# Performance work log

Measured on AMD Instinct MI355X. Metric: run time of the kernel, lower is better.

Reference implementation:

```python
import jax, jax.numpy as jnp
import numpy as np

# Sizes from init_kwargs / input_specs
D_MODEL = 1024; D_INT = 64; KW = 32; B = 2; L = 4096
SAMPLING = np.array([5, 5, 2, 1, 1]); DILATIONS = np.array([1, 1, 2, 4, 8])
SUBHEADS = len(SAMPLING); HEADS = int(SAMPLING.sum())  # 5, 14
HEAD_OF_SUB = np.repeat(np.arange(SUBHEADS), SAMPLING)  # subhead index for each head
HEAD_DIL = np.repeat(DILATIONS, SAMPLING)                # dilation for each head


def _win_idx(dil):
    # centered dilated band, clipped at sequence edges -> [L, KW]
    offs = (np.arange(KW) - KW // 2) * dil
    return np.clip(np.arange(L)[:, None] + offs[None, :], 0, L - 1)

SUB_IDX = jnp.asarray(np.stack([_win_idx(d) for d in DILATIONS]))  # [SUBHEADS, L, KW]
HEAD_IDX = jnp.asarray(np.stack([_win_idx(d) for d in HEAD_DIL]))  # [HEADS, L, KW]


def setup_inputs() -> dict:
    rng = jax.random.key(0)
    ks = jax.random.split(rng, 9)
    n = lambda i, sh, sc=1.0: jax.random.normal(ks[i], sh, dtype=jnp.float32) * sc
    return dict(
        query=n(0, (B, L, D_MODEL)),
        key=n(1, (B, L, D_MODEL)),
        value=n(2, (B, L, D_MODEL)),
        Wq=n(3, (SUBHEADS, D_MODEL, D_INT), 0.02),
        bq=jnp.zeros((SUBHEADS, D_INT), jnp.float32),
        Wk=n(4, (SUBHEADS, D_MODEL, D_INT), 0.02),
        bk=jnp.zeros((SUBHEADS, D_INT), jnp.float32),
        Wv=n(5, (HEADS, D_MODEL, D_INT), 0.02),
        bv=jnp.zeros((HEADS, D_INT), jnp.float32),
        Ws=n(6, (HEADS, KW, KW), 0.05) + jnp.eye(KW, dtype=jnp.float32)[None],
        bs=jnp.zeros((HEADS, KW), jnp.float32),
        Wc=n(7, (HEADS * D_INT, D_MODEL), 0.02),
        bc=jnp.zeros((D_MODEL,), jnp.float32),
    )


def reference(query, key, value, Wq, bq, Wk, bk, Wv, bv, Ws, bs, Wc, bc):
    # per-subhead query/key projections: [S, B, L, Di]
    q = jnp.einsum('bld,sdi->sbli', query, Wq) + bq[:, None, None, :]
    k = jnp.einsum('bld,sdi->sbli', key, Wk) + bk[:, None, None, :]
    # per-head value projection: [H, B, L, Di]
    v = jnp.einsum('bld,hdi->hbli', value, Wv) + bv[:, None, None, :]
    # dilated banded key windows per subhead: [S, B, L, KW, Di]
    kw = jax.vmap(lambda kh, ix: kh[:, ix], in_axes=(0, 0))(k, SUB_IDX)
    # banded scores [S, B, L, KW]
    scores = jnp.einsum('sbli,sblki->sblk', q, kw) / jnp.sqrt(jnp.float32(D_INT))
    # supersample: replicate each subhead's scores to its heads -> [H, B, L, KW]
    scores_h = scores[HEAD_OF_SUB]
    # per-head positional supersampling linear on the score window
    sampled = jnp.einsum('hblk,hkm->hblm', scores_h, Ws) + bs[:, None, None, :]
    attn = jax.nn.softmax(sampled, axis=-1)
    # dilated value windows per head: [H, B, L, KW, Di]
    vw = jax.vmap(lambda vh, ix: vh[:, ix], in_axes=(0, 0))(v, HEAD_IDX)
    out = jnp.einsum('hblk,hblki->hbli', attn, vw)  # [H, B, L, Di]
    out = jnp.transpose(out, (1, 2, 0, 3)).reshape(B, L, HEADS * D_INT)
    return out @ Wc + bc  # [B, L, D_MODEL]
```

## Files before the change

### kernel.cpp

```cpp
#include <hip/hip_runtime.h>
#include <math.h>

#define D_MODEL 1024
#define D_INT   64
#define KW      32
#define L_SEQ   4096
#define SUBHEADS 5
#define HEADS   14
#define M_ROWS  8192
#define N_CAT   896
#define NQK     320

typedef unsigned short us;
typedef unsigned int   uu;
typedef __attribute__((ext_vector_type(2))) unsigned int uu2;
typedef __attribute__((ext_vector_type(4))) unsigned int uu4;
typedef __attribute__((ext_vector_type(8))) short bf16x8_t;
typedef __attribute__((ext_vector_type(4))) float f32x4_t;

__device__ __forceinline__ float u2f(uu u) {
    float f; __builtin_memcpy(&f, &u, 4); return f;
}
__device__ __forceinline__ float blo(uu u) { return u2f(u << 16); }
__device__ __forceinline__ float bhi(uu u) { return u2f(u & 0xffff0000u); }
__device__ __forceinline__ us f2b(float f) {
    uu u; __builtin_memcpy(&u, &f, 4);
    u += 0x7fffu + ((u >> 16) & 1u);
    return (us)(u >> 16);
}
__device__ __forceinline__ uu pack2(float a, float b) {
    return (uu)f2b(a) | ((uu)f2b(b) << 16);
}
__device__ __forceinline__ uu cvtpk(float a, float b) {
    uu r;
    asm("v_cvt_pk_bf16_f32 %0, %1, %2" : "=v"(r) : "v"(a), "v"(b));
    return r;
}
__device__ __forceinline__ void load16(void* lds, const void* g) {
    __builtin_amdgcn_global_load_lds(
        (const __attribute__((address_space(1))) unsigned int*)g,
        (__attribute__((address_space(3))) unsigned int*)lds, 16, 0, 0);
}
__device__ __forceinline__ int subhead_of(int h) {
    return (h < 5) ? 0 : (h < 10) ? 1 : (h < 12) ? 2 : (h == 12) ? 3 : 4;
}

#define CAST_BLK 3072
__global__ __launch_bounds__(256)
void prep_kernel(const float* __restrict__ q, const float* __restrict__ k,
                 const float* __restrict__ v,
                 const float* __restrict__ Wq, const float* __restrict__ Wk,
                 const float* __restrict__ Wv, const float* __restrict__ Wc,
                 us* __restrict__ Xq, us* __restrict__ Xk, us* __restrict__ Xv,
                 us* __restrict__ Wqt, us* __restrict__ Wkt,
                 us* __restrict__ Wvt, us* __restrict__ Wct)
{
    __shared__ float t[32][33];
    const int tid = threadIdx.x;
    const int b = blockIdx.x;

    if (b < CAST_BLK) {
        const int arr = b >> 10;
        const int blk = b & 1023;
        const f32x4_t* s = (const f32x4_t*)((arr == 0) ? q : (arr == 1) ? k : v);
        uu2* d = (uu2*)((arr == 0) ? Xq : (arr == 1) ? Xk : Xv);
        const int i0 = blk * 2048 + tid;
        f32x4_t xs[8];
#pragma unroll
        for (int kk = 0; kk < 8; kk++)
            xs[kk] = __builtin_nontemporal_load(&s[i0 + kk * 256]);
#pragma unroll
        for (int kk = 0; kk < 8; kk++) {
            uu2 o;
            o.x = cvtpk(xs[kk].x, xs[kk].y);
            o.y = cvtpk(xs[kk].z, xs[kk].w);
            d[i0 + kk * 256] = o;
        }
        return;
    }

    int g = b - CAST_BLK;
    const float* S; us* D; int K, N;
    if (g < 640) {
        if (g < 320) { S = Wq; D = Wqt; } else { S = Wk; D = Wkt; g -= 320; }
        K = 1024; N = 64;
    } else if (g < 1536) {
        g -= 640; S = Wv; D = Wvt; K = 1024; N = 64;
    } else {
        g -= 1536; S = Wc; D = Wct; K = 896; N = 1024;
    }
    const int nkx = K >> 5;
    const int kx = g % nkx;
    const int rest = g / nkx;
    const int ny = rest % (N >> 5);
    const int z  = rest / (N >> 5);
    const int k0 = kx * 32, n0 = ny * 32;
    S += (size_t)z * K * N;
    D += (size_t)z * K * N;
    const int tx = tid & 31, ty = tid >> 5;
#pragma unroll
    for (int r = 0; r < 32; r += 8)
        t[r + ty][tx] = __builtin_nontemporal_load(&S[(size_t)(k0 + r + ty) * N + n0 + tx]);
    __syncthreads();
#pragma unroll
    for (int r = 0; r < 32; r += 8)
        D[(size_t)(n0 + r + ty) * K + k0 + tx] = f2b(t[tx][r + ty]);
}

__device__ __forceinline__
void gemm64_core(const us* __restrict__ A, const us* __restrict__ Bt,
                 const float* __restrict__ bias, us* __restrict__ C,
                 int K, int ldC, int row0, int col0, us* As, us* Bs)
{
    const int tid = threadIdx.x, w = tid >> 6, lane = tid & 63;
    const int m = lane & 15, quad = lane >> 4;
    const int sr = lane >> 3;
    const int scs = (lane & 7) ^ sr;
    const int mrow0 = (w & 3) * 32, ncol0 = (w >> 2) * 32;

    f32x4_t z4 = {0.f, 0.f, 0.f, 0.f};
    f32x4_t acc[2][2] = {{z4, z4}, {z4, z4}};

    for (int k0 = 0; k0 < K; k0 += 64) {
#pragma unroll
        for (int p = 0; p < 2; p++) {
            const int r = w * 16 + p * 8 + sr;
            load16(&As[(w * 16 + p * 8) * 64], A + (size_t)(row0 + r) * K + k0 + scs * 8);
        }
        {
            const int r = w * 8 + sr;
            load16(&Bs[(w * 8) * 64], Bt + (size_t)(col0 + r) * K + k0 + scs * 8);
        }
        __syncthreads();
#pragma unroll
        for (int ks = 0; ks < 2; ks++) {
            const int slot = ((ks * 4 + quad) ^ (m & 7)) * 8;
            bf16x8_t a[2], b[2];
#pragma unroll
            for (int t = 0; t < 2; t++) {
                a[t] = *(const bf16x8_t*)&As[(mrow0 + t * 16 + m) * 64 + slot];
                b[t] = *(const bf16x8_t*)&Bs[(ncol0 + t * 16 + m) * 64 + slot];
            }
#pragma unroll
            for (int i = 0; i < 2; i++)
#pragma unroll
                for (int j = 0; j < 2; j++)
                    acc[i][j] = __builtin_amdgcn_mfma_f32_16x16x32_bf16(a[i], b[j], acc[i][j], 0, 0, 0);
        }
        __syncthreads();
    }

#pragma unroll
    for (int i = 0; i < 2; i++) {
        const int rbase = row0 + mrow0 + i * 16 + quad * 4;
#pragma unroll
        for (int j = 0; j < 2; j++) {
            const int col = col0 + ncol0 + j * 16 + m;
            const float bi = bias[col];
#pragma unroll
            for (int r = 0; r < 4; r++)
                C[(size_t)(rbase + r) * ldC + col] = f2b(acc[i][j][r] + bi);
        }
    }
}

__device__ __forceinline__
void gemm128_core(const us* __restrict__ A, const us* __restrict__ Bt,
                  const float* __restrict__ bias, void* __restrict__ Cv,
                  int K, int ldC, int outBf16, int row0, int col0,
                  us* As, us* Bs)
{
    const int tid = threadIdx.x, w = tid >> 6, lane = tid & 63;
    const int m = lane & 15, quad = lane >> 4;
    const int sr = lane >> 3;
    const int scs = (lane & 7) ^ sr;
    const int mrow0 = (w & 1) * 64, ncol0 = (w >> 1) * 32;

    f32x4_t z = {0.f, 0.f, 0.f, 0.f};
    f32x4_t acc[4][2] = {{z,z},{z,z},{z,z},{z,z}};

    for (int k0 = 0; k0 < K; k0 += 64) {
#pragma unroll
        for (int p = 0; p < 2; p++) {
            const int r = w * 16 + p * 8 + sr;
            load16(&As[(w * 16 + p * 8) * 64], A  + (size_t)(row0 + r) * K + k0 + scs * 8);
            load16(&Bs[(w * 16 + p * 8) * 64], Bt + (size_t)(col0 + r) * K + k0 + scs * 8);
        }
        __syncthreads();
#pragma unroll
        for (int ks = 0; ks < 2; ks++) {
            const int slot = ((ks * 4 + quad) ^ (m & 7)) * 8;
            bf16x8_t a[4], b[2];
#pragma unroll
            for (int t = 0; t < 4; t++)
                a[t] = *(const bf16x8_t*)&As[(mrow0 + t * 16 + m) * 64 + slot];
#pragma unroll
            for (int t = 0; t < 2; t++)
                b[t] = *(const bf16x8_t*)&Bs[(ncol0 + t * 16 + m) * 64 + slot];
#pragma unroll
            for (int i = 0; i < 4; i++)
#pragma unroll
                for (int j = 0; j < 2; j++)
                    acc[i][j] = __builtin_amdgcn_mfma_f32_16x16x32_bf16(a[i], b[j], acc[i][j], 0, 0, 0);
        }
        __syncthreads();
    }

#pragma unroll
    for (int i = 0; i < 4; i++) {
        const int rbase = row0 + mrow0 + i * 16 + quad * 4;
        if (outBf16) {
            us* Cb = (us*)Cv;
#pragma unroll
            for (int j = 0; j < 2; j++) {
                const int col = col0 + ncol0 + j * 16 + m;
                const float bi = bias[col];
#pragma unroll
                for (int r = 0; r < 4; r++)
                    Cb[(size_t)(rbase + r) * ldC + col] = f2b(acc[i][j][r] + bi);
            }
        } else {
            float* Cb = (float*)Cv;
#pragma unroll
            for (int j = 0; j < 2; j++) {
                const int col = col0 + ncol0 + j * 16 + m;
                const float bi = bias[col];
#pragma unroll
                for (int r = 0; r < 4; r++)
                    Cb[(size_t)(rbase + r) * ldC + col] = acc[i][j][r] + bi;
            }
        }
    }
}

__global__ __launch_bounds__(512)
void proj_kernel(const us* __restrict__ Xq, const us* __restrict__ Xk,
                 const us* __restrict__ Xv,
                 const us* __restrict__ Wqt, const us* __restrict__ Wkt,
                 const us* __restrict__ Wvt,
                 const float* __restrict__ bq, const float* __restrict__ bk,
                 const float* __restrict__ bv,
                 us* __restrict__ qbuf, us* __restrict__ kbuf,
                 us* __restrict__ vbuf)
{
    __shared__ us As[128 * 64];
    __shared__ us Bs[128 * 64];
    const int b = blockIdx.x;
    if (b < 448) {
        gemm128_core(Xv, Wvt, bv, vbuf, D_MODEL, N_CAT, 1,
                     (b & 63) << 7, (b >> 6) << 7, As, Bs);
    } else if (b < 704) {
        const int idx = b - 448;
        const int bx = idx & 63;
        const int rest = idx >> 6;
        const int cy = rest & 1, z = rest >> 1;
        gemm128_core(z ? Xk : Xq, z ? Wkt : Wqt, z ? bk : bq,
                     z ? kbuf : qbuf, D_MODEL, NQK, 1,
                     bx << 7, cy << 7, As, Bs);
    } else {
        const int idx = b - 704;
        const int bx = idx & 63;
        const int z  = idx >> 6;
        gemm64_core(z ? Xk : Xq, z ? Wkt : Wqt, z ? bk : bq,
                    z ? kbuf : qbuf, D_MODEL, NQK,
                    bx << 7, 256, As, Bs);
    }
}

__global__ __launch_bounds__(512)
void gemm_out(const us* __restrict__ ab, const us* __restrict__ Wct,
              const float* __restrict__ bc, float* __restrict__ out)
{
    __shared__ us As[128 * 64];
    __shared__ us Bs[128 * 64];
    gemm128_core(ab, Wct, bc, out, N_CAT, D_MODEL, 0,
                 (int)(blockIdx.x << 7), (int)(blockIdx.y << 7), As, Bs);
}

template<int ROWS>
__global__ __launch_bounds__(256)
void attn_kernel(const us* __restrict__ qb, const us* __restrict__ kb,
                 const us* __restrict__ vb,
                 const float* __restrict__ Ws, const float* __restrict__ bs,
                 us* __restrict__ ab, int hbase)
{
    __shared__ uu    kv[ROWS * 36];
    __shared__ uu    qslab[64 * 32];
    __shared__ float sab[64 * 36];

    constexpr int VT = (ROWS * 8 + 255) / 256;

    const int tid  = threadIdx.x;
    const int wave = tid >> 6;
    const int lane = tid & 63;
    const int j    = lane & 31;
    const int half = lane >> 5;
    const int h    = hbase + blockIdx.y;
    const int s    = subhead_of(h);
    const int ld   = (s <= 1) ? 0 : (s - 1);
    const int d    = 1 << ld;
    const int ml0  = blockIdx.x * 64;
    const int l0   = ml0 & 4095;
    const int bm   = ml0 - l0;
    const int W    = 64 + 31 * d;
    const int Bseg = W >> ld;

    const uu4* kg4 = (const uu4*)kb;
    const uu4* qg4 = (const uu4*)qb;
    for (int idx = tid; idx < W * 8; idx += 256) {
        int r = idx >> 3, c4 = idx & 7;
        int src = l0 - 16 * d + r;
        src = src < 0 ? 0 : (src > 4095 ? 4095 : src);
        int slot = (r & (d - 1)) * Bseg + (r >> ld);
        *(uu4*)&kv[slot * 36 + c4 * 4] = kg4[(size_t)(bm + src) * 40 + s * 8 + c4];
    }
#pragma unroll
    for (int it = 0; it < 2; it++) {
        const int idx = it * 256 + tid;
        const int r = idx >> 3, c4 = idx & 7;
        load16(&qslab[(it * 256 + wave * 64) * 4],
               &qg4[(size_t)(ml0 + r) * 40 + s * 8 + c4]);
    }

    const uu4* vg4 = (const uu4*)vb;
    uu4 vreg[VT];
#pragma unroll
    for (int it = 0; it < VT; it++) {
        const int idx = it * 256 + tid;
        if (idx < W * 8) {
            const int r = idx >> 3, c4 = idx & 7;
            int src = l0 - 16 * d + r;
            src = src < 0 ? 0 : (src > 4095 ? 4095 : src);
            vreg[it] = vg4[(size_t)(bm + src) * 112 + h * 8 + c4];
        }
    }
    __syncthreads();

#pragma unroll
    for (int i = 0; i < 8; i++) {
        const int p = wave * 16 + i * 2 + half;
        const int sb = (p & (d - 1)) * Bseg + (p >> ld);
        const uu4* k4 = (const uu4*)&kv[(sb + j) * 36];
        const uu4* q4 = (const uu4*)&qslab[p * 32];
        float acc = 0.f;
#pragma unroll
        for (int q = 0; q < 8; q++) {
            uu4 kd = k4[q];
            uu4 qd = q4[q];
            acc = fmaf(blo(kd.x), blo(qd.x), acc); acc = fmaf(bhi(kd.x), bhi(qd.x), acc);
            acc = fmaf(blo(kd.y), blo(qd.y), acc); acc = fmaf(bhi(kd.y), bhi(qd.y), acc);
            acc = fmaf(blo(kd.z), blo(qd.z), acc); acc = fmaf(bhi(kd.z), bhi(qd.z), acc);
            acc = fmaf(blo(kd.w), blo(qd.w), acc); acc = fmaf(bhi(kd.w), bhi(qd.w), acc);
        }
        sab[p * 36 + j] = acc * 0.125f;
    }
    __syncthreads();

#pragma unroll
    for (int it = 0; it < VT; it++) {
        const int idx = it * 256 + tid;
        if (idx < W * 8) {
            const int r = idx >> 3, c4 = idx & 7;
            const int slot = (r & (d - 1)) * Bseg + (r >> ld);
            *(uu4*)&kv[slot * 36 + c4 * 4] = vreg[it];
        }
    }
    float wsr[32];
#pragma unroll
    for (int k = 0; k < 32; k++) wsr[k] = Ws[(size_t)h * 1024 + k * 32 + j];
    const float bsv = bs[h * 32 + j];

#pragma unroll
    for (int i = 0; i < 8; i++) {
        const int p = wave * 16 + i * 2 + half;
        const float4* s4 = (const float4*)&sab[p * 36];
        float acc = bsv;
#pragma unroll
        for (int q = 0; q < 8; q++) {
            float4 v = s4[q];
            acc = fmaf(v.x, wsr[q * 4 + 0], acc);
            acc = fmaf(v.y, wsr[q * 4 + 1], acc);
            acc = fmaf(v.z, wsr[q * 4 + 2], acc);
            acc = fmaf(v.w, wsr[q * 4 + 3], acc);
        }
        float mx = acc;
#pragma unroll
        for (int off = 16; off > 0; off >>= 1) mx = fmaxf(mx, __shfl_xor(mx, off, 64));
        float ex = __expf(acc - mx);
        float sum = ex;
#pragma unroll
        for (int off = 16; off > 0; off >>= 1) sum += __shfl_xor(sum, off, 64);
        sab[p * 36 + j] = ex / sum;
    }
    __syncthreads();

    const int o = lane >> 3;
    const int c = lane & 7;
#pragma unroll
    for (int pass = 0; pass < 2; pass++) {
        const int p  = wave * 16 + pass * 8 + o;
        const int ml = ml0 + p;
        const int sbp = (p & (d - 1)) * Bseg + (p >> ld);
        float a0 = 0.f, a1 = 0.f, a2 = 0.f, a3 = 0.f;
        float a4 = 0.f, a5 = 0.f, a6 = 0.f, a7 = 0.f;
#pragma unroll
        for (int mg = 0; mg < 4; mg++) {
            const float4 wA = *(const float4*)&sab[p * 36 + mg * 8];
            const float4 wB = *(const float4*)&sab[p * 36 + mg * 8 + 4];
            const float at8[8] = {wA.x, wA.y, wA.z, wA.w, wB.x, wB.y, wB.z, wB.w};
#pragma unroll
            for (int m2 = 0; m2 < 8; m2++) {
                const float at = at8[m2];
                uu4 vd = *(const uu4*)&kv[(sbp + mg * 8 + m2) * 36 + c * 4];
                a0 = fmaf(blo(vd.x), at, a0); a1 = fmaf(bhi(vd.x), at, a1);
                a2 = fmaf(blo(vd.y), at, a2); a3 = fmaf(bhi(vd.y), at, a3);
                a4 = fmaf(blo(vd.z), at, a4); a5 = fmaf(bhi(vd.z), at, a5);
                a6 = fmaf(blo(vd.w), at, a6); a7 = fmaf(bhi(vd.w), at, a7);
            }
        }
        uu4 od;
        od.x = pack2(a0, a1); od.y = pack2(a2, a3);
        od.z = pack2(a4, a5); od.w = pack2(a6, a7);
        *(uu4*)&((uu*)ab)[(size_t)ml * 448 + h * 32 + c * 4] = od;
    }
}

extern "C" void kernel_launch(void* const* d_in, const int* in_sizes, int n_in,
                              void* d_out, int out_size, void* d_ws, size_t ws_size,
                              hipStream_t stream)
{
    const float* query = (const float*)d_in[0];
    const float* key   = (const float*)d_in[1];
    const float* value = (const float*)d_in[2];
    const float* Wq    = (const float*)d_in[3];
    const float* bq    = (const float*)d_in[4];
    const float* Wk    = (const float*)d_in[5];
    const float* bk    = (const float*)d_in[6];
    const float* Wv    = (const float*)d_in[7];
    const float* bv    = (const float*)d_in[8];
    const float* Ws    = (const float*)d_in[9];
    const float* bs    = (const float*)d_in[10];
    const float* Wc    = (const float*)d_in[11];
    const float* bc    = (const float*)d_in[12];
    float* out = (float*)d_out;

    us* w = (us*)d_ws;
    us* Xq  = w;
    us* ab  = w;
    us* Xk  = Xq  + (size_t)M_ROWS * D_MODEL;
    us* Xv  = Xk  + (size_t)M_ROWS * D_MODEL;
    us* Wqt = Xv  + (size_t)M_ROWS * D_MODEL;
    us* Wkt = Wqt + (size_t)SUBHEADS * D_INT * D_MODEL;
    us* Wvt = Wkt + (size_t)SUBHEADS * D_INT * D_MODEL;
    us* Wct = Wvt + (size_t)HEADS * D_INT * D_MODEL;
    us* qbuf = Wct + (size_t)D_MODEL * N_CAT;
    us* kbuf = qbuf + (size_t)M_ROWS * NQK;
    us* vbuf = kbuf + (size_t)M_ROWS * NQK;

    dim3 blk(256);
    dim3 blk512(512);

    prep_kernel<<<dim3(CAST_BLK + 2432), blk, 0, stream>>>(
        query, key, value,
        Wq, Wk, Wv, Wc, Xq, Xk, Xv, Wqt, Wkt, Wvt, Wct);

    proj_kernel<<<dim3(832), blk512, 0, stream>>>(
        Xq, Xk, Xv, Wqt, Wkt, Wvt, bq, bk, bv, qbuf, kbuf, vbuf);

    attn_kernel<95><<<dim3(M_ROWS / 64, 10), blk, 0, stream>>>(
        qbuf, kbuf, vbuf, Ws, bs, ab, 0);
    attn_kernel<312><<<dim3(M_ROWS / 64, 4), blk, 0, stream>>>(
        qbuf, kbuf, vbuf, Ws, bs, ab, 10);

    gemm_out<<<dim3(M_ROWS / 128, D_MODEL / 128), blk512, 0, stream>>>(
        ab, Wct, bc, out);
}
```

Before: 262.0 us.

## Add MFMA-based banded attention kernel for dilation-1 heads

Adds a specialized attention kernel for the ten dilation-1 heads. It computes the banded QK scores with bf16 MFMA tiles over a contiguous 96-row key slab and keeps only the diagonal band entries. The value slab is prefetched into registers and written into shared memory that aliases the Q/K tiles. Some MFMA work is spent on out-of-band entries, which replaces the scalar per-row dot products of the generic kernel.

After: 254.2 us, median of 3. 3.0% less time.

```diff
diff --git a/kernel.cpp b/kernel.cpp
--- a/kernel.cpp
+++ b/kernel.cpp
@@ -277,6 +277,153 @@
                  (int)(blockIdx.x << 7), (int)(blockIdx.y << 7), As, Bs);
 }
 
+__global__ __launch_bounds__(256)
+void attn_d1_kernel(const us* __restrict__ qb, const us* __restrict__ kb,
+                    const us* __restrict__ vb,
+                    const float* __restrict__ Ws, const float* __restrict__ bs,
+                    us* __restrict__ ab)
+{
+    __shared__ us kq[96 * 64 + 64 * 64];
+    __shared__ float sab[64 * 36];
+
+    us* Ks = kq;
+    us* Qs = kq + 96 * 64;
+    uu* vslab = (uu*)kq;
+
+    const int tid  = threadIdx.x;
+    const int wave = tid >> 6;
+    const int lane = tid & 63;
+    const int m    = lane & 15, quad = lane >> 4;
+    const int sr   = lane >> 3;
+    const int scs  = (lane & 7) ^ sr;
+    const int j32  = lane & 31;
+    const int half = lane >> 5;
+    const int h    = blockIdx.y;
+    const int s    = (h < 5) ? 0 : 1;
+    const int ml0  = blockIdx.x * 64;
+    const int l0   = ml0 & 4095;
+    const int bm   = ml0 - l0;
+
+#pragma unroll
+    for (int call = 0; call < 3; call++) {
+        const int g = call * 4 + wave;
+        const int r = g * 8 + sr;
+        int src = l0 - 16 + r;
+        src = src < 0 ? 0 : (src > 4095 ? 4095 : src);
+        load16(&Ks[(g * 8) * 64], kb + (size_t)(bm + src) * NQK + s * 64 + scs * 8);
+    }
+#pragma unroll
+    for (int call = 0; call < 2; call++) {
+        const int g = call * 4 + wave;
+        const int r = g * 8 + sr;
+        load16(&Qs[(g * 8) * 64], qb + (size_t)(ml0 + r) * NQK + s * 64 + scs * 8);
+    }
+
+    const uu4* vg4 = (const uu4*)vb;
+    uu4 vreg[3];
+#pragma unroll
+    for (int it = 0; it < 3; it++) {
+        const int idx = it * 256 + tid;
+        if (idx < 95 * 8) {
+            const int r = idx >> 3, c4 = idx & 7;
+            int src = l0 - 16 + r;
+            src = src < 0 ? 0 : (src > 4095 ? 4095 : src);
+            vreg[it] = vg4[(size_t)(bm + src) * 112 + h * 8 + c4];
+        }
+    }
+    __syncthreads();
+
+    const int p0 = wave * 16;
+    f32x4_t z = {0.f, 0.f, 0.f, 0.f};
+    f32x4_t accs[3] = {z, z, z};
+#pragma unroll
+    for (int ks = 0; ks < 2; ks++) {
+        const int slot = ((ks * 4 + quad) ^ (m & 7)) * 8;
+        bf16x8_t qa = *(const bf16x8_t*)&Qs[(p0 + m) * 64 + slot];
+#pragma unroll
+        for (int wt = 0; wt < 3; wt++) {
+            bf16x8_t kb8 = *(const bf16x8_t*)&Ks[(p0 + wt * 16 + m) * 64 + slot];
+            accs[wt] = __builtin_amdgcn_mfma_f32_16x16x32_bf16(qa, kb8, accs[wt], 0, 0, 0);
+        }
+    }
+#pragma unroll
+    for (int wt = 0; wt < 3; wt++)
+#pragma unroll
+        for (int r = 0; r < 4; r++) {
+            const int ploc = quad * 4 + r;
+            const int j = wt * 16 + m - ploc;
+            if (j >= 0 && j < 32)
+                sab[(p0 + ploc) * 36 + j] = accs[wt][r] * 0.125f;
+        }
+    __syncthreads();
+
+#pragma unroll
+    for (int it = 0; it < 3; it++) {
+        const int idx = it * 256 + tid;
+        if (idx < 95 * 8) {
+            const int r = idx >> 3, c4 = idx & 7;
+            *(uu4*)&vslab[r * 36 + c4 * 4] = vreg[it];
+        }
+    }
+    float wsr[32];
+#pragma unroll
+    for (int k = 0; k < 32; k++) wsr[k] = Ws[(size_t)h * 1024 + k * 32 + j32];
+    const float bsv = bs[h * 32 + j32];
+
+#pragma unroll
+    for (int i = 0; i < 8; i++) {
+        const int p = wave * 16 + i * 2 + half;
+        const float4* s4 = (const float4*)&sab[p * 36];
+        float acc = bsv;
+#pragma unroll
+        for (int q = 0; q < 8; q++) {
+            float4 v = s4[q];
+            acc = fmaf(v.x, wsr[q * 4 + 0], acc);
+            acc = fmaf(v.y, wsr[q * 4 + 1], acc);
+            acc = fmaf(v.z, wsr[q * 4 + 2], acc);
+            acc = fmaf(v.w, wsr[q * 4 + 3], acc);
+        }
+        float mx = acc;
+#pragma unroll
+        for (int off = 16; off > 0; off >>= 1) mx = fmaxf(mx, __shfl_xor(mx, off, 64));
+        float ex = __expf(acc - mx);
+        float sum = ex;
+#pragma unroll
+        for (int off = 16; off > 0; off >>= 1) sum += __shfl_xor(sum, off, 64);
+        sab[p * 36 + j32] = ex / sum;
+    }
+    __syncthreads();
+
+    const int o = lane >> 3;
+    const int c = lane & 7;
+#pragma unroll
+    for (int pass = 0; pass < 2; pass++) {
+        const int p  = wave * 16 + pass * 8 + o;
+        const int ml = ml0 + p;
+        float a0 = 0.f, a1 = 0.f, a2 = 0.f, a3 = 0.f;
+        float a4 = 0.f, a5 = 0.f, a6 = 0.f, a7 = 0.f;
+#pragma unroll
+        for (int mg = 0; mg < 4; mg++) {
+            const float4 wA = *(const float4*)&sab[p * 36 + mg * 8];
+            const float4 wB = *(const float4*)&sab[p * 36 + mg * 8 + 4];
+            const float at8[8] = {wA.x, wA.y, wA.z, wA.w, wB.x, wB.y, wB.z, wB.w};
+#pragma unroll
+            for (int m2 = 0; m2 < 8; m2++) {
+                const float at = at8[m2];
+                uu4 vd = *(const uu4*)&vslab[(p + mg * 8 + m2) * 36 + c * 4];
+                a0 = fmaf(blo(vd.x), at, a0); a1 = fmaf(bhi(vd.x), at, a1);
+                a2 = fmaf(blo(vd.y), at, a2); a3 = fmaf(bhi(vd.y), at, a3);
+                a4 = fmaf(blo(vd.z), at, a4); a5 = fmaf(bhi(vd.z), at, a5);
+                a6 = fmaf(blo(vd.w), at, a6); a7 = fmaf(bhi(vd.w), at, a7);
+            }
+        }
+        uu4 od;
+        od.x = pack2(a0, a1); od.y = pack2(a2, a3);
+        od.z = pack2(a4, a5); od.w = pack2(a6, a7);
+        *(uu4*)&((uu*)ab)[(size_t)ml * 448 + h * 32 + c * 4] = od;
+    }
+}
+
 template<int ROWS>
 __global__ __launch_bounds__(256)
 void attn_kernel(const us* __restrict__ qb, const us* __restrict__ kb,
@@ -467,8 +614,8 @@
     proj_kernel<<<dim3(832), blk512, 0, stream>>>(
         Xq, Xk, Xv, Wqt, Wkt, Wvt, bq, bk, bv, qbuf, kbuf, vbuf);
 
-    attn_kernel<95><<<dim3(M_ROWS / 64, 10), blk, 0, stream>>>(
-        qbuf, kbuf, vbuf, Ws, bs, ab, 0);
+    attn_d1_kernel<<<dim3(M_ROWS / 64, 10), blk, 0, stream>>>(
+        qbuf, kbuf, vbuf, Ws, bs, ab);
     attn_kernel<312><<<dim3(M_ROWS / 64, 4), blk, 0, stream>>>(
         qbuf, kbuf, vbuf, Ws, bs, ab, 10);
 
```
